# Optimization experiments

Hardware: AMD Instinct MI355X
Metric: run time of the kernel (lower is better)

The kernel has to match this reference:

```python
import jax, jax.numpy as jnp
import numpy as np

B, S, D, H = 4, 2048, 1024, 16
HD = D // H


def setup_inputs() -> dict:
    key = jax.random.key(0)
    ks = jax.random.split(key, 5)
    scale = 1.0 / np.sqrt(D)
    inp = {
        "x": jax.random.normal(ks[0], (B, S, D), dtype=jnp.float32),
        # causal mask; masked_fill where mask == 0
        "mask": jnp.tril(jnp.ones((S, S), dtype=jnp.int32))[None, None, :, :],
        "Wq": jax.random.normal(ks[1], (D, D), dtype=jnp.float32) * scale,
        "bq": jnp.zeros((D,), dtype=jnp.float32),
        "Wk": jax.random.normal(ks[2], (D, D), dtype=jnp.float32) * scale,
        "bk": jnp.zeros((D,), dtype=jnp.float32),
        "Wv": jax.random.normal(ks[3], (D, D), dtype=jnp.float32) * scale,
        "bv": jnp.zeros((D,), dtype=jnp.float32),
        "Wo": jax.random.normal(ks[4], (D, D), dtype=jnp.float32) * scale,
        "bo": jnp.zeros((D,), dtype=jnp.float32),
    }
    return inp


def reference(x, mask, Wq, bq, Wk, bk, Wv, bv, Wo, bo):
    # weights stored [in, out]: y = x @ W + b (equivalent to torch Linear)
    def split_heads(t):  # [B,S,D] -> [B,H,S,HD]
        return t.reshape(B, S, H, HD).transpose(0, 2, 1, 3)

    q = split_heads(x @ Wq + bq)
    k = split_heads(x @ Wk + bk)
    v = split_heads(x @ Wv + bv)

    scores = jnp.einsum("bhqd,bhkd->bhqk", q, k) / jnp.sqrt(jnp.float32(HD))
    scores = jnp.where(mask == 0, -jnp.inf, scores)
    weights = jax.nn.softmax(scores, axis=-1)  # dropout_prob == 0, no dropout
    z = jnp.einsum("bhqk,bhkd->bhqd", weights, v)
    z = z.transpose(0, 2, 1, 3).reshape(B, S, D)
    return z @ Wo + bo
```

## Files before the change

kernel.cpp:

```cpp
#include <hip/hip_runtime.h>
#include <cmath>


#define BB 4
#define SS 2048
#define DD 1024
#define HH 16
#define HD 64
#define MM (BB * SS)

typedef __bf16 bf16x8 __attribute__((ext_vector_type(8)));
typedef float f32x4 __attribute__((ext_vector_type(4)));
typedef unsigned short ushort4e __attribute__((ext_vector_type(4)));
typedef unsigned short ushort8e __attribute__((ext_vector_type(8)));

#define SCALE_Q 0.18033688011112042f
#define EXP2(x) __builtin_amdgcn_exp2f(x)

__device__ __forceinline__ void gload_lds16(const void* g, void* l) {
    __builtin_amdgcn_global_load_lds((const __attribute__((address_space(1))) void*)g,
                                     (__attribute__((address_space(3))) void*)l, 16, 0, 0);
}

__device__ __forceinline__ unsigned short f2bf(float f) {
    union { float f; unsigned u; } v; v.f = f;
    unsigned r = v.u + 0x7fff + ((v.u >> 16) & 1);
    return (unsigned short)(r >> 16);
}

__global__ __launch_bounds__(256) void cast_f32_bf16(const float* __restrict__ in,
                                                     unsigned short* __restrict__ out) {
    const int i = blockIdx.x * 256 + threadIdx.x;
    const float4 v = ((const float4*)in)[i];
    ushort4e o;
    o[0] = f2bf(v.x); o[1] = f2bf(v.y); o[2] = f2bf(v.z); o[3] = f2bf(v.w);
    *(ushort4e*)&out[(size_t)i * 4] = o;
}

__global__ __launch_bounds__(256) void wtrans(const float* __restrict__ W0, const float* __restrict__ W1,
                                              const float* __restrict__ W2, const float* __restrict__ W3,
                                              unsigned short* __restrict__ O0, unsigned short* __restrict__ O1,
                                              unsigned short* __restrict__ O2, unsigned short* __restrict__ O3) {
    __shared__ unsigned short T[64][72];
    const float* W = blockIdx.z == 0 ? W0 : blockIdx.z == 1 ? W1 : blockIdx.z == 2 ? W2 : W3;
    unsigned short* O = blockIdx.z == 0 ? O0 : blockIdx.z == 1 ? O1 : blockIdx.z == 2 ? O2 : O3;
    const int k0 = blockIdx.x * 64, n0 = blockIdx.y * 64;
    const int t = threadIdx.x;
#pragma unroll
    for (int i = 0; i < 4; i++) {
        const int r = (t >> 4) + 16 * i, c4 = (t & 15) * 4;
        const float4 w = *(const float4*)&W[(size_t)(k0 + r) * DD + n0 + c4];
        T[c4 + 0][r] = f2bf(w.x); T[c4 + 1][r] = f2bf(w.y);
        T[c4 + 2][r] = f2bf(w.z); T[c4 + 3][r] = f2bf(w.w);
    }
    __syncthreads();
    const int nl = t >> 2, kc = (t & 3) * 16;
    const ushort8e a = *(const ushort8e*)&T[nl][kc];
    const ushort8e b = *(const ushort8e*)&T[nl][kc + 8];
    *(ushort8e*)&O[(size_t)(n0 + nl) * DD + k0 + kc] = a;
    *(ushort8e*)&O[(size_t)(n0 + nl) * DD + k0 + kc + 8] = b;
}

__global__ __launch_bounds__(256) void gemm_qkv(const unsigned short* __restrict__ A,
                                                const unsigned short* __restrict__ Bt,
                                                const float* __restrict__ bqp,
                                                const float* __restrict__ bkp,
                                                const float* __restrict__ bvp,
                                                unsigned short* __restrict__ qo,
                                                unsigned short* __restrict__ ko,
                                                unsigned short* __restrict__ vo) {
    __shared__ unsigned short As[2][4096];
    __shared__ unsigned short Bs[2][4096];
    const int tid = threadIdx.x, lane = tid & 63, w = tid >> 6;
    const int wm = w >> 1, wn = w & 1;
    const int g = lane >> 4, l15 = lane & 15;
    const int m0 = blockIdx.x * 128, n0 = blockIdx.y * 128;

    f32x4 acc[4][4];
#pragma unroll
    for (int i = 0; i < 4; i++)
#pragma unroll
        for (int j = 0; j < 4; j++) acc[i][j] = (f32x4){0.f, 0.f, 0.f, 0.f};

    const int ob0 = w * 2048, ob1 = w * 2048 + 1024;
    auto stage = [&](int bb, int k0) {
#pragma unroll
        for (int i = 0; i < 2; i++) {
            const int ob = i ? ob1 : ob0;
            const int o = ob + lane * 16;
            const int row = o >> 6;
            const int c = ((o >> 4) & 3) ^ (row & 3);
            gload_lds16(A + (size_t)(m0 + row) * DD + k0 + c * 8, (char*)&As[bb][0] + ob);
            gload_lds16(Bt + (size_t)(n0 + row) * DD + k0 + c * 8, (char*)&Bs[bb][0] + ob);
        }
    };

    int cur = 0;
    stage(0, 0);
    __syncthreads();
#pragma unroll 2
    for (int ks = 0; ks < 32; ks++) {
        if (ks + 1 < 32) stage(cur ^ 1, (ks + 1) * 32);
        bf16x8 af[4], bf[4];
#pragma unroll
        for (int mf = 0; mf < 4; mf++) {
            const int row = wm * 64 + mf * 16 + l15;
            const int c = g ^ (row & 3);
            af[mf] = *(const bf16x8*)((const char*)&As[cur][0] + row * 64 + c * 16);
        }
#pragma unroll
        for (int nf = 0; nf < 4; nf++) {
            const int row = wn * 64 + nf * 16 + l15;
            const int c = g ^ (row & 3);
            bf[nf] = *(const bf16x8*)((const char*)&Bs[cur][0] + row * 64 + c * 16);
        }
#pragma unroll
        for (int mf = 0; mf < 4; mf++)
#pragma unroll
            for (int nf = 0; nf < 4; nf++)
                acc[mf][nf] = __builtin_amdgcn_mfma_f32_16x16x32_bf16(af[mf], bf[nf], acc[mf][nf], 0, 0, 0);
        __syncthreads();
        cur ^= 1;
    }

    const int proj = n0 >> 10;
    const int nbase = n0 & 1023;
    const float* bias = proj == 0 ? bqp : proj == 1 ? bkp : bvp;
    unsigned short* op = proj == 0 ? qo : proj == 1 ? ko : vo;
    const float scale = proj == 0 ? SCALE_Q : 1.0f;
#pragma unroll
    for (int nf = 0; nf < 4; nf++) {
        const int col = nbase + wn * 64 + nf * 16 + l15;
        const float bv_ = bias[col];
        const int h = col >> 6, hd = col & 63;
#pragma unroll
        for (int mf = 0; mf < 4; mf++) {
            const int mrow0 = m0 + wm * 64 + mf * 16 + g * 4;
            const f32x4 v = acc[mf][nf];
            if (proj < 2) {
#pragma unroll
                for (int r = 0; r < 4; r++) {
                    const int m = mrow0 + r, b_ = m >> 11, s = m & 2047;
                    op[(((size_t)(b_ * HH + h)) * SS + s) * HD + hd] = f2bf((v[r] + bv_) * scale);
                }
            } else {
                const int m = mrow0, b_ = m >> 11, s = m & 2047;
                const int u = s & 63;
                const int pos = (s & ~63) + (u >> 5) * 32 + ((u >> 2) & 3) * 8 + ((u >> 4) & 1) * 4;
                ushort4e o4;
#pragma unroll
                for (int r = 0; r < 4; r++) o4[r] = f2bf(v[r] + bv_);
                *(ushort4e*)&op[(((size_t)(b_ * HH + h)) * HD + hd) * SS + pos] = o4;
            }
        }
    }
}

__global__ __launch_bounds__(256) void gemm_out(const unsigned short* __restrict__ A,
                                                const unsigned short* __restrict__ Bt,
                                                const float* __restrict__ bias,
                                                float* __restrict__ out) {
    __shared__ unsigned short As[2][4096];
    __shared__ unsigned short Bs[2][4096];
    const int tid = threadIdx.x, lane = tid & 63, w = tid >> 6;
    const int wm = w >> 1, wn = w & 1;
    const int g = lane >> 4, l15 = lane & 15;
    const int m0 = blockIdx.x * 128, n0 = blockIdx.y * 128;

    f32x4 acc[4][4];
#pragma unroll
    for (int i = 0; i < 4; i++)
#pragma unroll
        for (int j = 0; j < 4; j++) acc[i][j] = (f32x4){0.f, 0.f, 0.f, 0.f};

    const int ob0 = w * 2048, ob1 = w * 2048 + 1024;
    auto stage = [&](int bb, int k0) {
#pragma unroll
        for (int i = 0; i < 2; i++) {
            const int ob = i ? ob1 : ob0;
            const int o = ob + lane * 16;
            const int row = o >> 6;
            const int c = ((o >> 4) & 3) ^ (row & 3);
            gload_lds16(A + (size_t)(m0 + row) * DD + k0 + c * 8, (char*)&As[bb][0] + ob);
            gload_lds16(Bt + (size_t)(n0 + row) * DD + k0 + c * 8, (char*)&Bs[bb][0] + ob);
        }
    };

    int cur = 0;
    stage(0, 0);
    __syncthreads();
#pragma unroll 2
    for (int ks = 0; ks < 32; ks++) {
        if (ks + 1 < 32) stage(cur ^ 1, (ks + 1) * 32);
        bf16x8 af[4], bf[4];
#pragma unroll
        for (int mf = 0; mf < 4; mf++) {
            const int row = wm * 64 + mf * 16 + l15;
            const int c = g ^ (row & 3);
            af[mf] = *(const bf16x8*)((const char*)&As[cur][0] + row * 64 + c * 16);
        }
#pragma unroll
        for (int nf = 0; nf < 4; nf++) {
            const int row = wn * 64 + nf * 16 + l15;
            const int c = g ^ (row & 3);
            bf[nf] = *(const bf16x8*)((const char*)&Bs[cur][0] + row * 64 + c * 16);
        }
#pragma unroll
        for (int mf = 0; mf < 4; mf++)
#pragma unroll
            for (int nf = 0; nf < 4; nf++)
                acc[mf][nf] = __builtin_amdgcn_mfma_f32_16x16x32_bf16(af[mf], bf[nf], acc[mf][nf], 0, 0, 0);
        __syncthreads();
        cur ^= 1;
    }

#pragma unroll
    for (int nf = 0; nf < 4; nf++) {
        const int col = n0 + wn * 64 + nf * 16 + l15;
        const float bv_ = bias[col];
#pragma unroll
        for (int mf = 0; mf < 4; mf++) {
            const int mrow0 = m0 + wm * 64 + mf * 16 + g * 4;
            const f32x4 v = acc[mf][nf];
#pragma unroll
            for (int r = 0; r < 4; r++) out[(size_t)(mrow0 + r) * DD + col] = v[r] + bv_;
        }
    }
}

__global__ __launch_bounds__(256) void attn(const unsigned short* __restrict__ Q,
                                            const unsigned short* __restrict__ K,
                                            const unsigned short* __restrict__ Vt,
                                            unsigned short* __restrict__ Z) {
    __shared__ unsigned short Ks[2][4096];
    __shared__ unsigned short Vs[2][4096];

    const int tid = threadIdx.x, lane = tid & 63, w = tid >> 6;
    const int g = lane >> 4, l15 = lane & 15;
    const int bh = blockIdx.y, b = bh >> 4, h = bh & 15;
    const unsigned short* Qb = Q + (size_t)bh * SS * HD;
    const unsigned short* Kb = K + (size_t)bh * SS * HD;
    const unsigned short* Vb = Vt + (size_t)bh * HD * SS;

    const int ob0 = w * 2048, ob1 = w * 2048 + 1024;
    auto stage = [&](int bb, int kt) {
        const int k0 = kt * 64;
#pragma unroll
        for (int i = 0; i < 2; i++) {
            const int ob = i ? ob1 : ob0;
            const int o = ob + lane * 16;
            const int row = o >> 7;
            const int c = ((o >> 4) & 7) ^ (row & 7);
            gload_lds16(Kb + (size_t)(k0 + row) * HD + c * 8, (char*)&Ks[bb][0] + ob);
            gload_lds16(Vb + (size_t)row * SS + k0 + c * 8, (char*)&Vs[bb][0] + ob);
        }
    };

#pragma unroll
    for (int half = 0; half < 2; half++) {
        const int t = half ? (15 - blockIdx.x) : blockIdx.x;
        const int q0 = t * 128;
        const int qw = q0 + w * 32;

        bf16x8 qf[2][2];
#pragma unroll
        for (int nf = 0; nf < 2; nf++)
#pragma unroll
            for (int ks = 0; ks < 2; ks++)
                qf[nf][ks] = *(const bf16x8*)&Qb[(size_t)(qw + nf * 16 + l15) * HD + ks * 32 + g * 8];

        float m_[2] = {-INFINITY, -INFINITY}, ps[2] = {0.f, 0.f};
        f32x4 oacc[4][2];
#pragma unroll
        for (int mh = 0; mh < 4; mh++)
#pragma unroll
            for (int nf = 0; nf < 2; nf++) oacc[mh][nf] = (f32x4){0.f, 0.f, 0.f, 0.f};

        const int nt = 2 * t + 2;
        int cur = 0;
        stage(0, 0);
        __syncthreads();
#pragma unroll 2
        for (int kt = 0; kt < nt; kt++) {
            const int k0 = kt * 64;
            if (kt + 1 < nt) stage(cur ^ 1, kt + 1);
            if (k0 <= qw + 31) {
                f32x4 sacc[4][2];
#pragma unroll
                for (int mf = 0; mf < 4; mf++)
#pragma unroll
                    for (int nf = 0; nf < 2; nf++) sacc[mf][nf] = (f32x4){0.f, 0.f, 0.f, 0.f};
#pragma unroll
                for (int ks = 0; ks < 2; ks++) {
                    bf16x8 af[4];
#pragma unroll
                    for (int mf = 0; mf < 4; mf++) {
                        const int row = mf * 16 + l15;
                        const int c = (ks * 4 + g) ^ (row & 7);
                        af[mf] = *(const bf16x8*)((const char*)&Ks[cur][0] + row * 128 + c * 16);
                    }
#pragma unroll
                    for (int mf = 0; mf < 4; mf++)
#pragma unroll
                        for (int nf = 0; nf < 2; nf++)
                            sacc[mf][nf] = __builtin_amdgcn_mfma_f32_16x16x32_bf16(af[mf], qf[nf][ks], sacc[mf][nf], 0, 0, 0);
                }
                if (k0 + 63 > qw) {
#pragma unroll
                    for (int mf = 0; mf < 4; mf++)
#pragma unroll
                        for (int nf = 0; nf < 2; nf++)
#pragma unroll
                            for (int r = 0; r < 4; r++) {
                                const int key = k0 + mf * 16 + g * 4 + r;
                                const int q = qw + nf * 16 + l15;
                                if (key > q) sacc[mf][nf][r] = -INFINITY;
                            }
                }
                float pm[2];
#pragma unroll
                for (int nf = 0; nf < 2; nf++) {
                    float v = sacc[0][nf][0];
#pragma unroll
                    for (int mf = 0; mf < 4; mf++)
#pragma unroll
                        for (int r = 0; r < 4; r++) v = fmaxf(v, sacc[mf][nf][r]);
                    v = fmaxf(v, __shfl_xor(v, 16));
                    v = fmaxf(v, __shfl_xor(v, 32));
                    pm[nf] = v;
                }
                if (__any((pm[0] > m_[0] + 8.f) || (pm[1] > m_[1] + 8.f))) {
#pragma unroll
                    for (int nf = 0; nf < 2; nf++) {
                        const float mn = fmaxf(m_[nf], pm[nf]);
                        const float al = EXP2(m_[nf] - mn);
                        m_[nf] = mn;
                        ps[nf] *= al;
#pragma unroll
                        for (int mh = 0; mh < 4; mh++) oacc[mh][nf] *= al;
                    }
                }
                bf16x8 pb[2][2];
#pragma unroll
                for (int nf = 0; nf < 2; nf++) {
                    float pv[16];
#pragma unroll
                    for (int mf = 0; mf < 4; mf++)
#pragma unroll
                        for (int r = 0; r < 4; r++) {
                            const float p = EXP2(sacc[mf][nf][r] - m_[nf]);
                            pv[mf * 4 + r] = p;
                            ps[nf] += p;
                        }
#pragma unroll
                    for (int j = 0; j < 4; j++) {
                        pb[nf][0][j] = (__bf16)pv[j];
                        pb[nf][0][4 + j] = (__bf16)pv[4 + j];
                        pb[nf][1][j] = (__bf16)pv[8 + j];
                        pb[nf][1][4 + j] = (__bf16)pv[12 + j];
                    }
                }
#pragma unroll
                for (int ks = 0; ks < 2; ks++) {
#pragma unroll
                    for (int mh = 0; mh < 4; mh++) {
                        const int row = mh * 16 + l15;
                        const int c = (ks * 4 + g) ^ (row & 7);
                        const bf16x8 va = *(const bf16x8*)((const char*)&Vs[cur][0] + row * 128 + c * 16);
#pragma unroll
                        for (int nf = 0; nf < 2; nf++)
                            oacc[mh][nf] = __builtin_amdgcn_mfma_f32_16x16x32_bf16(va, pb[nf][ks], oacc[mh][nf], 0, 0, 0);
                    }
                }
            }
            __syncthreads();
            cur ^= 1;
        }

#pragma unroll
        for (int nf = 0; nf < 2; nf++) {
            float l = ps[nf];
            l += __shfl_xor(l, 16);
            l += __shfl_xor(l, 32);
            const float inv = 1.f / l;
            const int qg = qw + nf * 16 + l15;
#pragma unroll
            for (int mh = 0; mh < 4; mh++) {
                ushort4e o;
#pragma unroll
                for (int r = 0; r < 4; r++) o[r] = f2bf(oacc[mh][nf][r] * inv);
                *(ushort4e*)&Z[((size_t)(b * SS + qg)) * DD + h * HD + mh * 16 + g * 4] = o;
            }
        }
    }
}

extern "C" void kernel_launch(void* const* d_in, const int* in_sizes, int n_in,
                              void* d_out, int out_size, void* d_ws, size_t ws_size,
                              hipStream_t stream) {
    const float* x  = (const float*)d_in[0];
    const float* Wq = (const float*)d_in[2];
    const float* bq = (const float*)d_in[3];
    const float* Wk = (const float*)d_in[4];
    const float* bk = (const float*)d_in[5];
    const float* Wv = (const float*)d_in[6];
    const float* bv = (const float*)d_in[7];
    const float* Wo = (const float*)d_in[8];
    const float* bo = (const float*)d_in[9];
    float* out = (float*)d_out;

    unsigned short* xb  = (unsigned short*)d_ws;
    unsigned short* wqt = xb  + (size_t)MM * DD;
    unsigned short* wkt = wqt + (size_t)DD * DD;
    unsigned short* wvt = wkt + (size_t)DD * DD;
    unsigned short* wot = wvt + (size_t)DD * DD;
    unsigned short* qb  = wot + (size_t)DD * DD;
    unsigned short* kb  = qb  + (size_t)MM * DD;
    unsigned short* vtb = kb  + (size_t)MM * DD;
    unsigned short* zb  = vtb + (size_t)MM * DD;

    const dim3 blk(256);
    cast_f32_bf16<<<dim3(MM * DD / 1024), blk, 0, stream>>>(x, xb);
    wtrans<<<dim3(16, 16, 4), blk, 0, stream>>>(Wq, Wk, Wv, Wo, wqt, wkt, wvt, wot);

    gemm_qkv<<<dim3(MM / 128, 3 * DD / 128), blk, 0, stream>>>(xb, wqt, bq, bk, bv, qb, kb, vtb);

    attn<<<dim3(8, BB * HH), blk, 0, stream>>>(qb, kb, vtb, zb);

    gemm_out<<<dim3(MM / 128, DD / 128), blk, 0, stream>>>(zb, wot, bo, out);
}
```

Before: 292.9 us.

## Replace QKV and output GEMMs with 256x256-tile, 4-stage pipelined template kernel

```diff
diff --git a/kernel.cpp b/kernel.cpp
--- a/kernel.cpp
+++ b/kernel.cpp
@@ -61,169 +61,154 @@
     *(ushort8e*)&O[(size_t)(n0 + nl) * DD + k0 + kc + 8] = b;
 }
 
-__global__ __launch_bounds__(256) void gemm_qkv(const unsigned short* __restrict__ A,
-                                                const unsigned short* __restrict__ Bt,
-                                                const float* __restrict__ bqp,
-                                                const float* __restrict__ bkp,
-                                                const float* __restrict__ bvp,
-                                                unsigned short* __restrict__ qo,
-                                                unsigned short* __restrict__ ko,
-                                                unsigned short* __restrict__ vo) {
-    __shared__ unsigned short As[2][4096];
-    __shared__ unsigned short Bs[2][4096];
+template <int MODE>
+__global__ __launch_bounds__(512, 2) void gemm256(const unsigned short* __restrict__ A,
+                                                  const unsigned short* __restrict__ Bt,
+                                                  const float* __restrict__ b0,
+                                                  const float* __restrict__ b1,
+                                                  const float* __restrict__ b2,
+                                                  void* __restrict__ o0,
+                                                  void* __restrict__ o1,
+                                                  void* __restrict__ o2) {
+    __shared__ unsigned short Al[4][8192];
+    __shared__ unsigned short Bl[4][8192];
+
     const int tid = threadIdx.x, lane = tid & 63, w = tid >> 6;
-    const int wm = w >> 1, wn = w & 1;
+    const int wm = w >> 2, wn = w & 3;
     const int g = lane >> 4, l15 = lane & 15;
-    const int m0 = blockIdx.x * 128, n0 = blockIdx.y * 128;
-
-    f32x4 acc[4][4];
-#pragma unroll
-    for (int i = 0; i < 4; i++)
+    const int m0 = blockIdx.x * 256, n0 = blockIdx.y * 256;
+
+    f32x4 acc[8][4];
+#pragma unroll
+    for (int i = 0; i < 8; i++)
 #pragma unroll
         for (int j = 0; j < 4; j++) acc[i][j] = (f32x4){0.f, 0.f, 0.f, 0.f};
 
-    const int ob0 = w * 2048, ob1 = w * 2048 + 1024;
-    auto stage = [&](int bb, int k0) {
-#pragma unroll
-        for (int i = 0; i < 2; i++) {
-            const int ob = i ? ob1 : ob0;
-            const int o = ob + lane * 16;
-            const int row = o >> 6;
-            const int c = ((o >> 4) & 3) ^ (row & 3);
-            gload_lds16(A + (size_t)(m0 + row) * DD + k0 + c * 8, (char*)&As[bb][0] + ob);
-            gload_lds16(Bt + (size_t)(n0 + row) * DD + k0 + c * 8, (char*)&Bs[bb][0] + ob);
+    auto stageA = [&](int bb, int kt) {
+        const int k0 = kt * 32;
+#pragma unroll
+        for (int ld = 0; ld < 2; ld++) {
+            const int o = tid * 16 + ld * 8192;
+            const int r = o >> 6;
+            const int cc = ((o >> 4) & 3) ^ ((r >> 1) & 3);
+            gload_lds16(A + (size_t)(m0 + r) * DD + k0 + cc * 8,
+                        (char*)&Al[bb][0] + w * 1024 + ld * 8192);
         }
     };
-
-    int cur = 0;
-    stage(0, 0);
-    __syncthreads();
-#pragma unroll 2
-    for (int ks = 0; ks < 32; ks++) {
-        if (ks + 1 < 32) stage(cur ^ 1, (ks + 1) * 32);
-        bf16x8 af[4], bf[4];
+    auto stageB = [&](int bb, int kt) {
+        const int k0 = kt * 32;
+#pragma unroll
+        for (int ld = 0; ld < 2; ld++) {
+            const int o = tid * 16 + ld * 8192;
+            const int r = o >> 6;
+            const int cc = ((o >> 4) & 3) ^ ((r >> 1) & 3);
+            gload_lds16(Bt + (size_t)(n0 + r) * DD + k0 + cc * 8,
+                        (char*)&Bl[bb][0] + w * 1024 + ld * 8192);
+        }
+    };
+
+    stageA(0, 0); stageB(0, 0);
+    stageA(1, 1); stageB(1, 1);
+    stageA(2, 2); stageB(2, 2);
+    asm volatile("s_waitcnt vmcnt(8)" ::: "memory");
+    __builtin_amdgcn_s_barrier();
+
+    for (int kt = 0; kt < 32; kt++) {
+        const int bb = kt & 3;
+        const bool st = (kt <= 28);
+        bf16x8 bfr[4], afr[4];
+#pragma unroll
+        for (int nf = 0; nf < 4; nf++) {
+            const int r = wn * 64 + nf * 16 + l15;
+            bfr[nf] = *(const bf16x8*)((const char*)&Bl[bb][0] + r * 64 + ((g ^ ((r >> 1) & 3)) << 4));
+        }
 #pragma unroll
         for (int mf = 0; mf < 4; mf++) {
-            const int row = wm * 64 + mf * 16 + l15;
-            const int c = g ^ (row & 3);
-            af[mf] = *(const bf16x8*)((const char*)&As[cur][0] + row * 64 + c * 16);
-        }
+            const int r = wm * 128 + mf * 16 + l15;
+            afr[mf] = *(const bf16x8*)((const char*)&Al[bb][0] + r * 64 + ((g ^ ((r >> 1) & 3)) << 4));
+        }
+        if (st) stageA((kt + 3) & 3, kt + 3);
+        __builtin_amdgcn_s_barrier();
+        asm volatile("s_waitcnt lgkmcnt(0)" ::: "memory");
+        __builtin_amdgcn_sched_barrier(0);
+        __builtin_amdgcn_s_setprio(1);
+#pragma unroll
+        for (int mf = 0; mf < 4; mf++)
+#pragma unroll
+            for (int nf = 0; nf < 4; nf++)
+                acc[mf][nf] = __builtin_amdgcn_mfma_f32_16x16x32_bf16(afr[mf], bfr[nf], acc[mf][nf], 0, 0, 0);
+        __builtin_amdgcn_s_setprio(0);
+        __builtin_amdgcn_sched_barrier(0);
+        __builtin_amdgcn_s_barrier();
+        bf16x8 afr2[4];
+#pragma unroll
+        for (int mf = 0; mf < 4; mf++) {
+            const int r = wm * 128 + (mf + 4) * 16 + l15;
+            afr2[mf] = *(const bf16x8*)((const char*)&Al[bb][0] + r * 64 + ((g ^ ((r >> 1) & 3)) << 4));
+        }
+        if (st) stageB((kt + 3) & 3, kt + 3);
+        __builtin_amdgcn_s_barrier();
+        asm volatile("s_waitcnt lgkmcnt(0)" ::: "memory");
+        __builtin_amdgcn_sched_barrier(0);
+        __builtin_amdgcn_s_setprio(1);
+#pragma unroll
+        for (int mf = 0; mf < 4; mf++)
+#pragma unroll
+            for (int nf = 0; nf < 4; nf++)
+                acc[mf + 4][nf] = __builtin_amdgcn_mfma_f32_16x16x32_bf16(afr2[mf], bfr[nf], acc[mf + 4][nf], 0, 0, 0);
+        __builtin_amdgcn_s_setprio(0);
+        __builtin_amdgcn_sched_barrier(0);
+        if (kt <= 28) asm volatile("s_waitcnt vmcnt(8)" ::: "memory");
+        else if (kt == 29) asm volatile("s_waitcnt vmcnt(4)" ::: "memory");
+        else asm volatile("s_waitcnt vmcnt(0)" ::: "memory");
+        __builtin_amdgcn_s_barrier();
+    }
+
+    if (MODE == 1) {
+        float* op = (float*)o0;
 #pragma unroll
         for (int nf = 0; nf < 4; nf++) {
-            const int row = wn * 64 + nf * 16 + l15;
-            const int c = g ^ (row & 3);
-            bf[nf] = *(const bf16x8*)((const char*)&Bs[cur][0] + row * 64 + c * 16);
-        }
-#pragma unroll
-        for (int mf = 0; mf < 4; mf++)
-#pragma unroll
-            for (int nf = 0; nf < 4; nf++)
-                acc[mf][nf] = __builtin_amdgcn_mfma_f32_16x16x32_bf16(af[mf], bf[nf], acc[mf][nf], 0, 0, 0);
-        __syncthreads();
-        cur ^= 1;
-    }
-
-    const int proj = n0 >> 10;
-    const int nbase = n0 & 1023;
-    const float* bias = proj == 0 ? bqp : proj == 1 ? bkp : bvp;
-    unsigned short* op = proj == 0 ? qo : proj == 1 ? ko : vo;
-    const float scale = proj == 0 ? SCALE_Q : 1.0f;
-#pragma unroll
-    for (int nf = 0; nf < 4; nf++) {
-        const int col = nbase + wn * 64 + nf * 16 + l15;
-        const float bv_ = bias[col];
-        const int h = col >> 6, hd = col & 63;
-#pragma unroll
-        for (int mf = 0; mf < 4; mf++) {
-            const int mrow0 = m0 + wm * 64 + mf * 16 + g * 4;
-            const f32x4 v = acc[mf][nf];
-            if (proj < 2) {
-#pragma unroll
-                for (int r = 0; r < 4; r++) {
-                    const int m = mrow0 + r, b_ = m >> 11, s = m & 2047;
-                    op[(((size_t)(b_ * HH + h)) * SS + s) * HD + hd] = f2bf((v[r] + bv_) * scale);
-                }
-            } else {
-                const int m = mrow0, b_ = m >> 11, s = m & 2047;
-                const int u = s & 63;
-                const int pos = (s & ~63) + (u >> 5) * 32 + ((u >> 2) & 3) * 8 + ((u >> 4) & 1) * 4;
-                ushort4e o4;
-#pragma unroll
-                for (int r = 0; r < 4; r++) o4[r] = f2bf(v[r] + bv_);
-                *(ushort4e*)&op[(((size_t)(b_ * HH + h)) * HD + hd) * SS + pos] = o4;
+            const int col = n0 + wn * 64 + nf * 16 + l15;
+            const float bv_ = b0[col];
+#pragma unroll
+            for (int mf = 0; mf < 8; mf++) {
+                const int mrow0 = m0 + wm * 128 + mf * 16 + g * 4;
+                const f32x4 v = acc[mf][nf];
+#pragma unroll
+                for (int r = 0; r < 4; r++) op[(size_t)(mrow0 + r) * DD + col] = v[r] + bv_;
             }
         }
-    }
-}
-
-__global__ __launch_bounds__(256) void gemm_out(const unsigned short* __restrict__ A,
-                                                const unsigned short* __restrict__ Bt,
-                                                const float* __restrict__ bias,
-                                                float* __restrict__ out) {
-    __shared__ unsigned short As[2][4096];
-    __shared__ unsigned short Bs[2][4096];
-    const int tid = threadIdx.x, lane = tid & 63, w = tid >> 6;
-    const int wm = w >> 1, wn = w & 1;
-    const int g = lane >> 4, l15 = lane & 15;
-    const int m0 = blockIdx.x * 128, n0 = blockIdx.y * 128;
-
-    f32x4 acc[4][4];
-#pragma unroll
-    for (int i = 0; i < 4; i++)
-#pragma unroll
-        for (int j = 0; j < 4; j++) acc[i][j] = (f32x4){0.f, 0.f, 0.f, 0.f};
-
-    const int ob0 = w * 2048, ob1 = w * 2048 + 1024;
-    auto stage = [&](int bb, int k0) {
-#pragma unroll
-        for (int i = 0; i < 2; i++) {
-            const int ob = i ? ob1 : ob0;
-            const int o = ob + lane * 16;
-            const int row = o >> 6;
-            const int c = ((o >> 4) & 3) ^ (row & 3);
-            gload_lds16(A + (size_t)(m0 + row) * DD + k0 + c * 8, (char*)&As[bb][0] + ob);
-            gload_lds16(Bt + (size_t)(n0 + row) * DD + k0 + c * 8, (char*)&Bs[bb][0] + ob);
-        }
-    };
-
-    int cur = 0;
-    stage(0, 0);
-    __syncthreads();
-#pragma unroll 2
-    for (int ks = 0; ks < 32; ks++) {
-        if (ks + 1 < 32) stage(cur ^ 1, (ks + 1) * 32);
-        bf16x8 af[4], bf[4];
-#pragma unroll
-        for (int mf = 0; mf < 4; mf++) {
-            const int row = wm * 64 + mf * 16 + l15;
-            const int c = g ^ (row & 3);
-            af[mf] = *(const bf16x8*)((const char*)&As[cur][0] + row * 64 + c * 16);
-        }
+    } else {
+        const int proj = n0 >> 10;
+        const int nbase = n0 & 1023;
+        const float* bias = proj == 0 ? b0 : proj == 1 ? b1 : b2;
+        unsigned short* op = (unsigned short*)(proj == 0 ? o0 : proj == 1 ? o1 : o2);
+        const float scale = proj == 0 ? SCALE_Q : 1.0f;
 #pragma unroll
         for (int nf = 0; nf < 4; nf++) {
-            const int row = wn * 64 + nf * 16 + l15;
-            const int c = g ^ (row & 3);
-            bf[nf] = *(const bf16x8*)((const char*)&Bs[cur][0] + row * 64 + c * 16);
-        }
-#pragma unroll
-        for (int mf = 0; mf < 4; mf++)
-#pragma unroll
-            for (int nf = 0; nf < 4; nf++)
-                acc[mf][nf] = __builtin_amdgcn_mfma_f32_16x16x32_bf16(af[mf], bf[nf], acc[mf][nf], 0, 0, 0);
-        __syncthreads();
-        cur ^= 1;
-    }
-
-#pragma unroll
-    for (int nf = 0; nf < 4; nf++) {
-        const int col = n0 + wn * 64 + nf * 16 + l15;
-        const float bv_ = bias[col];
-#pragma unroll
-        for (int mf = 0; mf < 4; mf++) {
-            const int mrow0 = m0 + wm * 64 + mf * 16 + g * 4;
-            const f32x4 v = acc[mf][nf];
-#pragma unroll
-            for (int r = 0; r < 4; r++) out[(size_t)(mrow0 + r) * DD + col] = v[r] + bv_;
+            const int col = nbase + wn * 64 + nf * 16 + l15;
+            const float bv_ = bias[col];
+            const int h = col >> 6, hd = col & 63;
+#pragma unroll
+            for (int mf = 0; mf < 8; mf++) {
+                const int mrow0 = m0 + wm * 128 + mf * 16 + g * 4;
+                const f32x4 v = acc[mf][nf];
+                if (proj < 2) {
+#pragma unroll
+                    for (int r = 0; r < 4; r++) {
+                        const int m = mrow0 + r, b_ = m >> 11, s = m & 2047;
+                        op[(((size_t)(b_ * HH + h)) * SS + s) * HD + hd] = f2bf((v[r] + bv_) * scale);
+                    }
+                } else {
+                    const int m = mrow0, b_ = m >> 11, s = m & 2047;
+                    const int u = s & 63;
+                    const int pos = (s & ~63) + (u >> 5) * 32 + ((u >> 2) & 3) * 8 + ((u >> 4) & 1) * 4;
+                    ushort4e o4;
+#pragma unroll
+                    for (int r = 0; r < 4; r++) o4[r] = f2bf(v[r] + bv_);
+                    *(ushort4e*)&op[(((size_t)(b_ * HH + h)) * HD + hd) * SS + pos] = o4;
+                }
+            }
         }
     }
 }
@@ -419,13 +404,13 @@
     unsigned short* vtb = kb  + (size_t)MM * DD;
     unsigned short* zb  = vtb + (size_t)MM * DD;
 
-    const dim3 blk(256);
+    const dim3 blk(256), blk2(512);
     cast_f32_bf16<<<dim3(MM * DD / 1024), blk, 0, stream>>>(x, xb);
     wtrans<<<dim3(16, 16, 4), blk, 0, stream>>>(Wq, Wk, Wv, Wo, wqt, wkt, wvt, wot);
 
-    gemm_qkv<<<dim3(MM / 128, 3 * DD / 128), blk, 0, stream>>>(xb, wqt, bq, bk, bv, qb, kb, vtb);
+    gemm256<0><<<dim3(MM / 256, 3 * DD / 256), blk2, 0, stream>>>(xb, wqt, bq, bk, bv, qb, kb, vtb);
 
     attn<<<dim3(8, BB * HH), blk, 0, stream>>>(qb, kb, vtb, zb);
 
-    gemm_out<<<dim3(MM / 128, DD / 128), blk, 0, stream>>>(zb, wot, bo, out);
-}
+    gemm256<1><<<dim3(MM / 256, DD / 256), blk2, 0, stream>>>(zb, wot, bo, bo, bo, out, out, out);
+}
```

After: 298.4 us. About the same (+1.9%).
